# Optimization experiments

Hardware: AMD Instinct MI355X
Metric: run time of the kernel (lower is better)

The kernel has to match this reference:

```python
import jax, jax.numpy as jnp
import numpy as np

N = 131072      # num nodes
T = 16          # tile (block) size, tile_rows == tile_cols
BR = N // T     # block rows = 8192
K = 8           # nonzero blocks per block-row
IN_F, HID, NCLS = 128, 256, 64
LN_EPS = 1e-5


def setup_inputs() -> dict:
    key = jax.random.key(0)
    ks = jax.random.split(key, 8)
    features = jax.random.normal(ks[0], (N, IN_F), dtype=jnp.float32)
    block_vals = jax.random.uniform(ks[1], (BR, K, T, T), dtype=jnp.float32) / (K * T)
    block_cols = jax.random.randint(ks[2], (BR, K), 0, BR, dtype=jnp.int32)
    W0 = jax.random.normal(ks[3], (IN_F, HID), dtype=jnp.float32) / np.sqrt(IN_F)
    W1 = jax.random.normal(ks[4], (HID, HID), dtype=jnp.float32) / np.sqrt(HID)
    W2 = jax.random.normal(ks[5], (HID, NCLS), dtype=jnp.float32) / np.sqrt(HID)
    return {
        "features": features,
        "block_vals": block_vals,
        "W0": W0, "b0": jnp.zeros((HID,), jnp.float32),
        "W1": W1, "b1": jnp.zeros((HID,), jnp.float32),
        "W2": W2, "b2": jnp.zeros((NCLS,), jnp.float32),
        "g0": jnp.ones((HID,), jnp.float32), "beta0": jnp.zeros((HID,), jnp.float32),
        "g1": jnp.ones((HID,), jnp.float32), "beta1": jnp.zeros((HID,), jnp.float32),
        "block_cols": block_cols,
    }


def bcsr_spmm(block_vals, block_cols, z):
    """Block-CSR sparse matmul: out = A @ z.
    block_vals: [BR, K, T, T], block_cols: [BR, K] (block-column ids), z: [N, F]."""
    f = z.shape[-1]
    zb = z.reshape(BR, T, f)[block_cols]          # gather column blocks -> [BR, K, T, F]
    out = jnp.einsum('bkrc,bkcf->brf', block_vals, zb)  # block GEMM + accumulate over K
    return out.reshape(N, f)


def layer_norm(x, g, b):
    mu = jnp.mean(x, axis=-1, keepdims=True)
    var = jnp.mean(jnp.square(x - mu), axis=-1, keepdims=True)
    return g * (x - mu) * jax.lax.rsqrt(var + LN_EPS) + b


def reference(features, block_vals, W0, b0, W1, b1, W2, b2,
              g0, beta0, g1, beta1, block_cols):
    # layer 0: h' = A @ (h W0) + b0 ; relu ; LayerNorm
    h = bcsr_spmm(block_vals, block_cols, features @ W0) + b0
    h = layer_norm(jax.nn.relu(h), g0, beta0)
    # layer 1
    h = bcsr_spmm(block_vals, block_cols, h @ W1) + b1
    h = layer_norm(jax.nn.relu(h), g1, beta1)
    # output layer (no activation/norm)
    h = bcsr_spmm(block_vals, block_cols, h @ W2) + b2
    return h
```

## Files before the change

### kernel.cpp

```cpp
#include <hip/hip_runtime.h>
#include <hip/hip_bf16.h>


typedef __bf16 bf16;
typedef bf16 bf16x8 __attribute__((ext_vector_type(8)));
typedef bf16 bf16x4 __attribute__((ext_vector_type(4)));
typedef float f32x4 __attribute__((ext_vector_type(4)));

#define N_NODES 131072
#define BRQ 8192
#define KNZ 8
#define IN_F 128
#define HID 256
#define NCLS 64

static __device__ __forceinline__ f32x4 mfma16(bf16x8 a, bf16x8 b, f32x4 c) {
  return __builtin_amdgcn_mfma_f32_16x16x32_bf16(a, b, c, 0, 0, 0);
}

static __device__ __forceinline__ bf16x8 load8(const bf16* p) {
  return *(const bf16x8*)p;
}
static __device__ __forceinline__ bf16x8 load8(const float* p) {
  f32x4 a0 = *(const f32x4*)p;
  f32x4 a1 = *(const f32x4*)(p + 4);
  bf16x8 r;
  r[0] = (bf16)a0[0]; r[1] = (bf16)a0[1]; r[2] = (bf16)a0[2]; r[3] = (bf16)a0[3];
  r[4] = (bf16)a1[0]; r[5] = (bf16)a1[1]; r[6] = (bf16)a1[2]; r[7] = (bf16)a1[3];
  return r;
}

__global__ void transpose_all(const float* __restrict__ W0, const float* __restrict__ W1,
                              const float* __restrict__ W2, bf16* __restrict__ w0t,
                              bf16* __restrict__ w1t, bf16* __restrict__ w2t) {
  int idx = blockIdx.x * 256 + threadIdx.x;
  if (idx < 32768) {
    int r = idx >> 8, c = idx & 255;
    w0t[c * 128 + r] = (bf16)W0[idx];
  } else if (idx < 98304) {
    int j = idx - 32768; int r = j >> 8, c = j & 255;
    w1t[c * 256 + r] = (bf16)W1[j];
  } else {
    int j = idx - 98304; int r = j >> 6, c = j & 63;
    w2t[c * 256 + r] = (bf16)W2[j];
  }
}

template<typename TA, int KIN, int FOUT, int GRID>
__global__ __launch_bounds__(256) void gemm_bt(const TA* __restrict__ X,
                                               const bf16* __restrict__ WT,
                                               bf16* __restrict__ Zbt) {
  constexpr int CG  = FOUT / 64;
  constexpr int KS  = KIN / 32;
  constexpr int RTS = GRID * 4 / CG;
  constexpr int NT  = BRQ / RTS;

  const int wave = threadIdx.x >> 6;
  const int lane = threadIdx.x & 63;
  const int l15  = lane & 15;
  const int quad = lane >> 4;
  const int gw   = blockIdx.x * 4 + wave;
  const int cg   = gw % CG;
  const int rt0  = gw / CG;

  const bf16* __restrict__ wbase = WT + (long)(cg * 64 + l15) * KIN + quad * 8;
  bf16x8 bfr[KS][4];
#pragma unroll
  for (int k = 0; k < KS; ++k)
#pragma unroll
    for (int t = 0; t < 4; ++t)
      bfr[k][t] = *(const bf16x8*)(wbase + t * (16 * KIN) + k * 32);

  const TA* __restrict__ xbase = X + (long)l15 * KIN + quad * 8;

  bf16x8 aw[2][KS];
#pragma unroll
  for (int k = 0; k < KS; ++k)
    aw[0][k] = load8(xbase + (long)rt0 * (16 * KIN) + k * 32);

#pragma unroll
  for (int it = 0; it < NT; ++it) {
    const int rt = rt0 + it * RTS;
    if (it + 1 < NT) {
      const long xoff = (long)(rt + RTS) * (16 * KIN);
#pragma unroll
      for (int k = 0; k < KS; ++k)
        aw[(it + 1) & 1][k] = load8(xbase + xoff + k * 32);
    }
    f32x4 acc[4] = {};
#pragma unroll
    for (int k = 0; k < KS; ++k)
#pragma unroll
      for (int t = 0; t < 4; ++t)
        acc[t] = mfma16(aw[it & 1][k], bfr[k][t], acc[t]);
#pragma unroll
    for (int t = 0; t < 4; ++t) {
      int col = cg * 64 + t * 16 + l15;
      bf16x4 v;
#pragma unroll
      for (int i = 0; i < 4; ++i) v[i] = (bf16)acc[t][i];
      *(bf16x4*)(Zbt + ((long)rt * FOUT + col) * 16 + quad * 4) = v;
    }
  }
}

__global__ __launch_bounds__(256) void spmm_ln(const float* __restrict__ Abv,
                                               const int*   __restrict__ Abc,
                                               const bf16*  __restrict__ Zbt,
                                               const float* __restrict__ bias,
                                               const float* __restrict__ gamma,
                                               const float* __restrict__ beta,
                                               bf16* __restrict__ H) {
  const int wave = threadIdx.x >> 6;
  const int lane = threadIdx.x & 63;
  const int l15  = lane & 15;
  const int quad = lane >> 4;
  const int b    = blockIdx.x * 2 + (wave >> 1);
  const int ch   = wave & 1;

  const int*   bc    = Abc + b * KNZ;
  const int    cst   = (quad & 1) * 8;
  const int    half  = quad >> 1;
  const float* abase = Abv + (long)b * (KNZ * 256) + l15 * 16 + cst;

  bf16x8 afr[4];
  long   zb[4];
#pragma unroll
  for (int kp = 0; kp < 4; ++kp) {
    int blk = 2 * kp + half;
    afr[kp] = load8(abase + blk * 256);
    zb[kp]  = (long)bc[blk] * (HID * 16) + cst;
  }
  bf16x8 bfr[4][8];
#pragma unroll
  for (int kp = 0; kp < 4; ++kp)
#pragma unroll
    for (int t = 0; t < 8; ++t) {
      int f = ch * 128 + t * 16 + l15;
      bfr[kp][t] = *(const bf16x8*)(Zbt + zb[kp] + f * 16);
    }

  f32x4 acc[8] = {};
#pragma unroll
  for (int kp = 0; kp < 4; ++kp)
#pragma unroll
    for (int t = 0; t < 8; ++t)
      acc[t] = mfma16(afr[kp], bfr[kp][t], acc[t]);

  float gv[8], bv[8];
#pragma unroll
  for (int t = 0; t < 8; ++t) {
    int f = ch * 128 + t * 16 + l15;
    gv[t] = gamma[f];
    bv[t] = beta[f];
  }
  float ps[4] = {0.f, 0.f, 0.f, 0.f}, pss[4] = {0.f, 0.f, 0.f, 0.f};
#pragma unroll
  for (int t = 0; t < 8; ++t) {
    float bi = bias[ch * 128 + t * 16 + l15];
#pragma unroll
    for (int i = 0; i < 4; ++i) {
      float v = acc[t][i] + bi;
      v = v > 0.f ? v : 0.f;
      acc[t][i] = v;
      ps[i] += v;
      pss[i] += v * v;
    }
  }
#pragma unroll
  for (int m = 1; m < 16; m <<= 1) {
#pragma unroll
    for (int i = 0; i < 4; ++i) {
      ps[i]  += __shfl_xor(ps[i], m, 64);
      pss[i] += __shfl_xor(pss[i], m, 64);
    }
  }
  __shared__ float S[4][16], SS[4][16];
  if (l15 == 0) {
#pragma unroll
    for (int i = 0; i < 4; ++i) {
      S[wave][quad * 4 + i]  = ps[i];
      SS[wave][quad * 4 + i] = pss[i];
    }
  }
  __syncthreads();
#pragma unroll
  for (int i = 0; i < 4; ++i) {
    int r = quad * 4 + i;
    float s    = S[wave][r] + S[wave ^ 1][r];
    float ss   = SS[wave][r] + SS[wave ^ 1][r];
    float mu   = s * (1.f / 256.f);
    float var  = ss * (1.f / 256.f) - mu * mu;
    float rstd = rsqrtf(var + 1e-5f);
    bf16* hrow = H + (long)(b * 16 + r) * HID;
#pragma unroll
    for (int t = 0; t < 8; ++t) {
      int f = ch * 128 + t * 16 + l15;
      float y = (acc[t][i] - mu) * rstd * gv[t] + bv[t];
      hrow[f] = (bf16)y;
    }
  }
}

__global__ __launch_bounds__(256) void spmm_out(const float* __restrict__ Abv,
                                                const int*   __restrict__ Abc,
                                                const bf16*  __restrict__ Zbt,
                                                const float* __restrict__ bias,
                                                float* __restrict__ out) {
  const int wave = threadIdx.x >> 6;
  const int b    = blockIdx.x * 4 + wave;
  const int lane = threadIdx.x & 63;
  const int l15  = lane & 15;
  const int quad = lane >> 4;

  const int*   bc    = Abc + b * KNZ;
  const int    cst   = (quad & 1) * 8;
  const int    half  = quad >> 1;
  const float* abase = Abv + (long)b * (KNZ * 256) + l15 * 16 + cst;

  bf16x8 afr[4];
  long   zb[4];
#pragma unroll
  for (int kp = 0; kp < 4; ++kp) {
    int blk = 2 * kp + half;
    afr[kp] = load8(abase + blk * 256);
    zb[kp]  = (long)bc[blk] * (NCLS * 16) + cst;
  }
  bf16x8 bfr[4][4];
#pragma unroll
  for (int kp = 0; kp < 4; ++kp)
#pragma unroll
    for (int t = 0; t < 4; ++t) {
      int f = t * 16 + l15;
      bfr[kp][t] = *(const bf16x8*)(Zbt + zb[kp] + f * 16);
    }

  f32x4 acc[4] = {};
#pragma unroll
  for (int kp = 0; kp < 4; ++kp)
#pragma unroll
    for (int t = 0; t < 4; ++t)
      acc[t] = mfma16(afr[kp], bfr[kp][t], acc[t]);

#pragma unroll
  for (int t = 0; t < 4; ++t) {
    int f = t * 16 + l15;
    float bi = bias[f];
#pragma unroll
    for (int i = 0; i < 4; ++i) {
      out[(long)(b * 16 + quad * 4 + i) * NCLS + f] = acc[t][i] + bi;
    }
  }
}

extern "C" void kernel_launch(void* const* d_in, const int* in_sizes, int n_in,
                              void* d_out, int out_size, void* d_ws, size_t ws_size,
                              hipStream_t stream) {
  const float* features = (const float*)d_in[0];
  const float* bvals    = (const float*)d_in[1];
  const float* W0       = (const float*)d_in[2];
  const float* b0       = (const float*)d_in[3];
  const float* W1       = (const float*)d_in[4];
  const float* b1       = (const float*)d_in[5];
  const float* W2       = (const float*)d_in[6];
  const float* b2       = (const float*)d_in[7];
  const float* g0       = (const float*)d_in[8];
  const float* beta0    = (const float*)d_in[9];
  const float* g1       = (const float*)d_in[10];
  const float* beta1    = (const float*)d_in[11];
  const int*   bcols    = (const int*)d_in[12];
  float* outp = (float*)d_out;

  bf16* zbt = (bf16*)d_ws;
  bf16* h   = zbt + (size_t)N_NODES * HID;

  bf16* w0t = (bf16*)d_out;
  bf16* w1t = w0t + IN_F * HID;
  bf16* w2t = w1t + HID * HID;

  transpose_all<<<dim3(448), dim3(256), 0, stream>>>(W0, W1, W2, w0t, w1t, w2t);

  gemm_bt<float, IN_F, HID, 1024><<<dim3(1024), dim3(256), 0, stream>>>(features, w0t, zbt);
  spmm_ln<<<dim3(BRQ / 2), dim3(256), 0, stream>>>(bvals, bcols, zbt, b0, g0, beta0, h);
  gemm_bt<bf16, HID, HID, 1024><<<dim3(1024), dim3(256), 0, stream>>>(h, w1t, zbt);
  spmm_ln<<<dim3(BRQ / 2), dim3(256), 0, stream>>>(bvals, bcols, zbt, b1, g1, beta1, h);
  gemm_bt<bf16, HID, NCLS, 512><<<dim3(512), dim3(256), 0, stream>>>(h, w2t, zbt);
  spmm_out<<<dim3(BRQ / 4), dim3(256), 0, stream>>>(bvals, bcols, zbt, b2, outp);
}
```

Before: 462.7 us.

## Reorder layer-0 as (A@X)@W0, pre-convert block values to bf16, fuse LayerNorm into GEMM

Layer 0 now runs the block-sparse product on the 128-wide features first, then multiplies by W0. Because A is linear this gives the same result, and the gather-heavy SpMM works on half the width. The sparse block values are converted to bf16 once into the output buffer and shared by all three SpMMs, so the fp32 values are no longer re-read in each layer. Bias, ReLU and LayerNorm are fused into the layer-0 GEMM epilogue using a cross-wave shared-memory reduction with a barrier per tile. The separate weight-transpose kernel is removed: weights are read strided from fp32 and converted inside each GEMM. The costs are extra prep kernels and more complex buffer aliasing.

Result: no change. 468.0 us (+1.1%).

```diff
diff --git a/kernel.cpp b/kernel.cpp
--- a/kernel.cpp
+++ b/kernel.cpp
@@ -14,6 +14,8 @@
 #define HID 256
 #define NCLS 64
 
+#define SB() __builtin_amdgcn_sched_barrier(0)
+
 static __device__ __forceinline__ f32x4 mfma16(bf16x8 a, bf16x8 b, f32x4 c) {
   return __builtin_amdgcn_mfma_f32_16x16x32_bf16(a, b, c, 0, 0, 0);
 }
@@ -21,34 +23,93 @@
 static __device__ __forceinline__ bf16x8 load8(const bf16* p) {
   return *(const bf16x8*)p;
 }
-static __device__ __forceinline__ bf16x8 load8(const float* p) {
-  f32x4 a0 = *(const f32x4*)p;
-  f32x4 a1 = *(const f32x4*)(p + 4);
+static __device__ __forceinline__ bf16x8 cvt8(f32x4 a0, f32x4 a1) {
   bf16x8 r;
   r[0] = (bf16)a0[0]; r[1] = (bf16)a0[1]; r[2] = (bf16)a0[2]; r[3] = (bf16)a0[3];
   r[4] = (bf16)a1[0]; r[5] = (bf16)a1[1]; r[6] = (bf16)a1[2]; r[7] = (bf16)a1[3];
   return r;
 }
 
-__global__ void transpose_all(const float* __restrict__ W0, const float* __restrict__ W1,
-                              const float* __restrict__ W2, bf16* __restrict__ w0t,
-                              bf16* __restrict__ w1t, bf16* __restrict__ w2t) {
-  int idx = blockIdx.x * 256 + threadIdx.x;
-  if (idx < 32768) {
-    int r = idx >> 8, c = idx & 255;
-    w0t[c * 128 + r] = (bf16)W0[idx];
-  } else if (idx < 98304) {
-    int j = idx - 32768; int r = j >> 8, c = j & 255;
-    w1t[c * 256 + r] = (bf16)W1[j];
-  } else {
-    int j = idx - 98304; int r = j >> 6, c = j & 63;
-    w2t[c * 256 + r] = (bf16)W2[j];
-  }
-}
-
-template<typename TA, int KIN, int FOUT, int GRID>
-__global__ __launch_bounds__(256) void gemm_bt(const TA* __restrict__ X,
-                                               const bf16* __restrict__ WT,
+__global__ __launch_bounds__(256) void prep_bvals(const float* __restrict__ V,
+                                                  bf16* __restrict__ Ab) {
+  long i = ((long)blockIdx.x * 256 + threadIdx.x) * 8;
+  f32x4 a0 = *(const f32x4*)(V + i);
+  f32x4 a1 = *(const f32x4*)(V + i + 4);
+  *(bf16x8*)(Ab + i) = cvt8(a0, a1);
+}
+
+__global__ __launch_bounds__(256) void prep_fbt(const float* __restrict__ F,
+                                                bf16* __restrict__ out) {
+  __shared__ float T[16][132];
+  const int b = blockIdx.x, tid = threadIdx.x;
+#pragma unroll
+  for (int p = 0; p < 2; ++p) {
+    int ci = tid + p * 256;
+    int r = ci >> 5, c4 = ci & 31;
+    f32x4 v = *(const f32x4*)(F + ((long)b * 16 + r) * 128 + c4 * 4);
+    *(f32x4*)&T[r][c4 * 4] = v;
+  }
+  __syncthreads();
+  int f = tid >> 1, r0 = (tid & 1) * 8;
+  bf16x8 o;
+#pragma unroll
+  for (int e = 0; e < 8; ++e) o[e] = (bf16)T[r0 + e][f];
+  *(bf16x8*)(out + (long)b * 2048 + f * 16 + r0) = o;
+}
+
+__global__ __launch_bounds__(256) void spmm_f(const bf16* __restrict__ Ab,
+                                              const int*  __restrict__ Abc,
+                                              const bf16* __restrict__ Fbt,
+                                              bf16* __restrict__ S0) {
+  const int wave = threadIdx.x >> 6;
+  const int b    = blockIdx.x * 4 + wave;
+  const int lane = threadIdx.x & 63;
+  const int l15  = lane & 15;
+  const int quad = lane >> 4;
+  const int cst  = (quad & 1) * 8;
+  const int half = quad >> 1;
+
+  const int*  bc    = Abc + b * KNZ;
+  const bf16* abase = Ab + (long)b * (KNZ * 256) + l15 * 16 + cst;
+
+  bf16x8 afr[4];
+  long   zb[4];
+#pragma unroll
+  for (int kp = 0; kp < 4; ++kp) {
+    int blk = 2 * kp + half;
+    afr[kp] = load8(abase + blk * 256);
+    zb[kp]  = (long)bc[blk] * (IN_F * 16) + cst;
+  }
+  bf16x8 bfr[4][8];
+#pragma unroll
+  for (int kp = 0; kp < 4; ++kp)
+#pragma unroll
+    for (int t = 0; t < 8; ++t) {
+      int f = t * 16 + l15;
+      bfr[kp][t] = *(const bf16x8*)(Fbt + zb[kp] + f * 16);
+    }
+
+  f32x4 acc[8] = {};
+#pragma unroll
+  for (int kp = 0; kp < 4; ++kp)
+#pragma unroll
+    for (int t = 0; t < 8; ++t)
+      acc[t] = mfma16(afr[kp], bfr[kp][t], acc[t]);
+
+#pragma unroll
+  for (int t = 0; t < 8; ++t)
+#pragma unroll
+    for (int i = 0; i < 4; ++i)
+      S0[((long)b * 16 + quad * 4 + i) * IN_F + t * 16 + l15] = (bf16)acc[t][i];
+}
+
+template<int KIN, int FOUT, int GRID, bool LN>
+__global__ __launch_bounds__(256) void gemm_ln(const bf16*  __restrict__ X,
+                                               const float* __restrict__ W,
+                                               const float* __restrict__ bias,
+                                               const float* __restrict__ gamma,
+                                               const float* __restrict__ beta,
+                                               bf16* __restrict__ Hrow,
                                                bf16* __restrict__ Zbt) {
   constexpr int CG  = FOUT / 64;
   constexpr int KS  = KIN / 32;
@@ -63,15 +124,29 @@
   const int cg   = gw % CG;
   const int rt0  = gw / CG;
 
-  const bf16* __restrict__ wbase = WT + (long)(cg * 64 + l15) * KIN + quad * 8;
-  bf16x8 bfr[KS][4];
+  bf16x8 wbf[KS][4];
 #pragma unroll
   for (int k = 0; k < KS; ++k)
 #pragma unroll
-    for (int t = 0; t < 4; ++t)
-      bfr[k][t] = *(const bf16x8*)(wbase + t * (16 * KIN) + k * 32);
-
-  const TA* __restrict__ xbase = X + (long)l15 * KIN + quad * 8;
+    for (int t = 0; t < 4; ++t) {
+      const float* wp = W + (long)(k * 32 + quad * 8) * FOUT + cg * 64 + t * 16 + l15;
+      bf16x8 v;
+#pragma unroll
+      for (int j = 0; j < 8; ++j) v[j] = (bf16)wp[(long)j * FOUT];
+      wbf[k][t] = v;
+    }
+  float bv[4], gv[4], btv[4];
+  if constexpr (LN) {
+#pragma unroll
+    for (int t = 0; t < 4; ++t) {
+      int col = cg * 64 + t * 16 + l15;
+      bv[t] = bias[col]; gv[t] = gamma[col]; btv[t] = beta[col];
+    }
+  }
+
+  __shared__ float S[2][4][16], SS[2][4][16];
+
+  const bf16* __restrict__ xbase = X + (long)l15 * KIN + quad * 8;
 
   bf16x8 aw[2][KS];
 #pragma unroll
@@ -92,19 +167,65 @@
     for (int k = 0; k < KS; ++k)
 #pragma unroll
       for (int t = 0; t < 4; ++t)
-        acc[t] = mfma16(aw[it & 1][k], bfr[k][t], acc[t]);
-#pragma unroll
-    for (int t = 0; t < 4; ++t) {
-      int col = cg * 64 + t * 16 + l15;
-      bf16x4 v;
-#pragma unroll
-      for (int i = 0; i < 4; ++i) v[i] = (bf16)acc[t][i];
-      *(bf16x4*)(Zbt + ((long)rt * FOUT + col) * 16 + quad * 4) = v;
-    }
-  }
-}
-
-__global__ __launch_bounds__(256) void spmm_ln(const float* __restrict__ Abv,
+        acc[t] = mfma16(aw[it & 1][k], wbf[k][t], acc[t]);
+
+    if constexpr (LN) {
+      float ps[4] = {0.f, 0.f, 0.f, 0.f}, pss[4] = {0.f, 0.f, 0.f, 0.f};
+#pragma unroll
+      for (int t = 0; t < 4; ++t)
+#pragma unroll
+        for (int i = 0; i < 4; ++i) {
+          float v = acc[t][i] + bv[t];
+          v = v > 0.f ? v : 0.f;
+          acc[t][i] = v;
+          ps[i] += v;
+          pss[i] += v * v;
+        }
+#pragma unroll
+      for (int m = 1; m < 16; m <<= 1)
+#pragma unroll
+        for (int i = 0; i < 4; ++i) {
+          ps[i]  += __shfl_xor(ps[i], m, 64);
+          pss[i] += __shfl_xor(pss[i], m, 64);
+        }
+      const int par = it & 1;
+      if (l15 == 0)
+#pragma unroll
+        for (int i = 0; i < 4; ++i) {
+          S[par][wave][quad * 4 + i]  = ps[i];
+          SS[par][wave][quad * 4 + i] = pss[i];
+        }
+      SB();
+      asm volatile("s_waitcnt lgkmcnt(0)" ::: "memory");
+      __builtin_amdgcn_s_barrier();
+      SB();
+#pragma unroll
+      for (int i = 0; i < 4; ++i) {
+        int r = quad * 4 + i;
+        float s  = S[par][0][r] + S[par][1][r] + S[par][2][r] + S[par][3][r];
+        float ss = SS[par][0][r] + SS[par][1][r] + SS[par][2][r] + SS[par][3][r];
+        float mu   = s * (1.f / FOUT);
+        float var  = ss * (1.f / FOUT) - mu * mu;
+        float rstd = rsqrtf(var + 1e-5f);
+        bf16* hrow = Hrow + ((long)rt * 16 + r) * FOUT + cg * 64;
+#pragma unroll
+        for (int t = 0; t < 4; ++t)
+          hrow[t * 16 + l15] = (bf16)((acc[t][i] - mu) * rstd * gv[t] + btv[t]);
+      }
+    } else {
+#pragma unroll
+      for (int t = 0; t < 4; ++t) {
+        int col = cg * 64 + t * 16 + l15;
+        bf16x4 v;
+#pragma unroll
+        for (int i = 0; i < 4; ++i) v[i] = (bf16)acc[t][i];
+        *(bf16x4*)(Zbt + ((long)rt * FOUT + col) * 16 + quad * 4) = v;
+      }
+    }
+  }
+}
+
+__global__ __launch_bounds__(256) void spmm_ln(const bf16*  __restrict__ Abv,
                                                const int*   __restrict__ Abc,
                                                const bf16*  __restrict__ Zbt,
                                                const float* __restrict__ bias,
@@ -118,10 +239,10 @@
   const int b    = blockIdx.x * 2 + (wave >> 1);
   const int ch   = wave & 1;
 
-  const int*   bc    = Abc + b * KNZ;
-  const int    cst   = (quad & 1) * 8;
-  const int    half  = quad >> 1;
-  const float* abase = Abv + (long)b * (KNZ * 256) + l15 * 16 + cst;
+  const int*  bc    = Abc + b * KNZ;
+  const int   cst   = (quad & 1) * 8;
+  const int   half  = quad >> 1;
+  const bf16* abase = Abv + (long)b * (KNZ * 256) + l15 * 16 + cst;
 
   bf16x8 afr[4];
   long   zb[4];
@@ -202,7 +323,7 @@
   }
 }
 
-__global__ __launch_bounds__(256) void spmm_out(const float* __restrict__ Abv,
+__global__ __launch_bounds__(256) void spmm_out(const bf16*  __restrict__ Abv,
                                                 const int*   __restrict__ Abc,
                                                 const bf16*  __restrict__ Zbt,
                                                 const float* __restrict__ bias,
@@ -213,10 +334,10 @@
   const int l15  = lane & 15;
   const int quad = lane >> 4;
 
-  const int*   bc    = Abc + b * KNZ;
-  const int    cst   = (quad & 1) * 8;
-  const int    half  = quad >> 1;
-  const float* abase = Abv + (long)b * (KNZ * 256) + l15 * 16 + cst;
+  const int*  bc    = Abc + b * KNZ;
+  const int   cst   = (quad & 1) * 8;
+  const int   half  = quad >> 1;
+  const bf16* abase = Abv + (long)b * (KNZ * 256) + l15 * 16 + cst;
 
   bf16x8 afr[4];
   long   zb[4];
@@ -259,11 +380,11 @@
   const float* features = (const float*)d_in[0];
   const float* bvals    = (const float*)d_in[1];
   const float* W0       = (const float*)d_in[2];
-  const float* b0       = (const float*)d_in[3];
+  const float* b0v      = (const float*)d_in[3];
   const float* W1       = (const float*)d_in[4];
-  const float* b1       = (const float*)d_in[5];
+  const float* b1v      = (const float*)d_in[5];
   const float* W2       = (const float*)d_in[6];
-  const float* b2       = (const float*)d_in[7];
+  const float* b2v      = (const float*)d_in[7];
   const float* g0       = (const float*)d_in[8];
   const float* beta0    = (const float*)d_in[9];
   const float* g1       = (const float*)d_in[10];
@@ -271,19 +392,26 @@
   const int*   bcols    = (const int*)d_in[12];
   float* outp = (float*)d_out;
 
-  bf16* zbt = (bf16*)d_ws;
-  bf16* h   = zbt + (size_t)N_NODES * HID;
-
-  bf16* w0t = (bf16*)d_out;
-  bf16* w1t = w0t + IN_F * HID;
-  bf16* w2t = w1t + HID * HID;
-
-  transpose_all<<<dim3(448), dim3(256), 0, stream>>>(W0, W1, W2, w0t, w1t, w2t);
-
-  gemm_bt<float, IN_F, HID, 1024><<<dim3(1024), dim3(256), 0, stream>>>(features, w0t, zbt);
-  spmm_ln<<<dim3(BRQ / 2), dim3(256), 0, stream>>>(bvals, bcols, zbt, b0, g0, beta0, h);
-  gemm_bt<bf16, HID, HID, 1024><<<dim3(1024), dim3(256), 0, stream>>>(h, w1t, zbt);
-  spmm_ln<<<dim3(BRQ / 2), dim3(256), 0, stream>>>(bvals, bcols, zbt, b1, g1, beta1, h);
-  gemm_bt<bf16, HID, NCLS, 512><<<dim3(512), dim3(256), 0, stream>>>(h, w2t, zbt);
-  spmm_out<<<dim3(BRQ / 4), dim3(256), 0, stream>>>(bvals, bcols, zbt, b2, outp);
-}
+  char* ws = (char*)d_ws;
+  bf16* fbt  = (bf16*)ws;
+  bf16* S0   = (bf16*)(ws + (64L << 20));
+  bf16* h0   = (bf16*)ws;
+  bf16* zbt1 = (bf16*)(ws + (64L << 20));
+  bf16* h1   = (bf16*)ws;
+  bf16* zbt2 = (bf16*)(ws + (64L << 20));
+
+  bf16* Ab = (bf16*)d_out;
+
+  prep_bvals<<<dim3(BRQ), dim3(256), 0, stream>>>(bvals, Ab);
+  prep_fbt<<<dim3(BRQ), dim3(256), 0, stream>>>(features, fbt);
+
+  spmm_f<<<dim3(BRQ / 4), dim3(256), 0, stream>>>(Ab, bcols, fbt, S0);
+  gemm_ln<IN_F, HID, 1024, true><<<dim3(1024), dim3(256), 0, stream>>>(
+      S0, W0, b0v, g0, beta0, h0, nullptr);
+  gemm_ln<HID, HID, 1024, false><<<dim3(1024), dim3(256), 0, stream>>>(
+      h0, W1, nullptr, nullptr, nullptr, nullptr, zbt1);
+  spmm_ln<<<dim3(BRQ / 2), dim3(256), 0, stream>>>(Ab, bcols, zbt1, b1v, g1, beta1, h1);
+  gemm_ln<HID, NCLS, 512, false><<<dim3(512), dim3(256), 0, stream>>>(
+      h1, W2, nullptr, nullptr, nullptr, nullptr, zbt2);
+  spmm_out<<<dim3(BRQ / 4), dim3(256), 0, stream>>>(Ab, bcols, zbt2, b2v, outp);
+}
```

## Convert adjacency blocks to bf16 once and fold weight transpose into GEMMs

Applied to the files above, without the earlier changes.

The fp32 block values are now converted to bf16 once, inside extra workgroups appended to the first GEMM launch, and stored in the output buffer. All three SpMM kernels then read the half-size bf16 copy instead of re-reading fp32, which cuts their memory traffic. The separate weight-transpose kernel is removed: each GEMM loads fp32 weights with strided reads and converts them in registers, saving one launch. The risks are spmm_out reading Ab from the same output buffer it writes (each wave overwrites only the region it has already read), and uncoalesced strided weight loads.

Result: slower. 490.3 us (+6.0%).

```diff
diff --git a/kernel.cpp b/kernel.cpp
--- a/kernel.cpp
+++ b/kernel.cpp
@@ -21,55 +21,47 @@
 static __device__ __forceinline__ bf16x8 load8(const bf16* p) {
   return *(const bf16x8*)p;
 }
-static __device__ __forceinline__ bf16x8 load8(const float* p) {
-  f32x4 a0 = *(const f32x4*)p;
-  f32x4 a1 = *(const f32x4*)(p + 4);
+static __device__ __forceinline__ bf16x8 cvt8(f32x4 a0, f32x4 a1) {
   bf16x8 r;
   r[0] = (bf16)a0[0]; r[1] = (bf16)a0[1]; r[2] = (bf16)a0[2]; r[3] = (bf16)a0[3];
   r[4] = (bf16)a1[0]; r[5] = (bf16)a1[1]; r[6] = (bf16)a1[2]; r[7] = (bf16)a1[3];
   return r;
 }
-
-__global__ void transpose_all(const float* __restrict__ W0, const float* __restrict__ W1,
-                              const float* __restrict__ W2, bf16* __restrict__ w0t,
-                              bf16* __restrict__ w1t, bf16* __restrict__ w2t) {
-  int idx = blockIdx.x * 256 + threadIdx.x;
-  if (idx < 32768) {
-    int r = idx >> 8, c = idx & 255;
-    w0t[c * 128 + r] = (bf16)W0[idx];
-  } else if (idx < 98304) {
-    int j = idx - 32768; int r = j >> 8, c = j & 255;
-    w1t[c * 256 + r] = (bf16)W1[j];
-  } else {
-    int j = idx - 98304; int r = j >> 6, c = j & 63;
-    w2t[c * 256 + r] = (bf16)W2[j];
-  }
+static __device__ __forceinline__ bf16x8 load8(const float* p) {
+  f32x4 a0 = *(const f32x4*)p;
+  f32x4 a1 = *(const f32x4*)(p + 4);
+  return cvt8(a0, a1);
 }
 
 template<typename TA, int KIN, int FOUT, int GRID>
-__global__ __launch_bounds__(256) void gemm_bt(const TA* __restrict__ X,
-                                               const bf16* __restrict__ WT,
-                                               bf16* __restrict__ Zbt) {
+static __device__ __forceinline__ void gemm_body(int wgid, int tid,
+                                                 const TA* __restrict__ X,
+                                                 const float* __restrict__ W,
+                                                 bf16* __restrict__ Zbt) {
   constexpr int CG  = FOUT / 64;
   constexpr int KS  = KIN / 32;
   constexpr int RTS = GRID * 4 / CG;
   constexpr int NT  = BRQ / RTS;
 
-  const int wave = threadIdx.x >> 6;
-  const int lane = threadIdx.x & 63;
+  const int wave = tid >> 6;
+  const int lane = tid & 63;
   const int l15  = lane & 15;
   const int quad = lane >> 4;
-  const int gw   = blockIdx.x * 4 + wave;
+  const int gw   = wgid * 4 + wave;
   const int cg   = gw % CG;
   const int rt0  = gw / CG;
 
-  const bf16* __restrict__ wbase = WT + (long)(cg * 64 + l15) * KIN + quad * 8;
-  bf16x8 bfr[KS][4];
+  bf16x8 wbf[KS][4];
 #pragma unroll
   for (int k = 0; k < KS; ++k)
 #pragma unroll
-    for (int t = 0; t < 4; ++t)
-      bfr[k][t] = *(const bf16x8*)(wbase + t * (16 * KIN) + k * 32);
+    for (int t = 0; t < 4; ++t) {
+      const float* wp = W + (long)(k * 32 + quad * 8) * FOUT + cg * 64 + t * 16 + l15;
+      bf16x8 v;
+#pragma unroll
+      for (int j = 0; j < 8; ++j) v[j] = (bf16)wp[(long)j * FOUT];
+      wbf[k][t] = v;
+    }
 
   const TA* __restrict__ xbase = X + (long)l15 * KIN + quad * 8;
 
@@ -92,7 +84,7 @@
     for (int k = 0; k < KS; ++k)
 #pragma unroll
       for (int t = 0; t < 4; ++t)
-        acc[t] = mfma16(aw[it & 1][k], bfr[k][t], acc[t]);
+        acc[t] = mfma16(aw[it & 1][k], wbf[k][t], acc[t]);
 #pragma unroll
     for (int t = 0; t < 4; ++t) {
       int col = cg * 64 + t * 16 + l15;
@@ -104,7 +96,29 @@
   }
 }
 
-__global__ __launch_bounds__(256) void spmm_ln(const float* __restrict__ Abv,
+__global__ __launch_bounds__(256) void gemm0_prep(const float* __restrict__ X,
+                                                  const float* __restrict__ W,
+                                                  bf16* __restrict__ Zbt,
+                                                  const float* __restrict__ V,
+                                                  bf16* __restrict__ Ab) {
+  if (blockIdx.x < 1024) {
+    gemm_body<float, IN_F, HID, 1024>(blockIdx.x, threadIdx.x, X, W, Zbt);
+  } else {
+    long i = ((long)(blockIdx.x - 1024) * 256 + threadIdx.x) * 8;
+    f32x4 a0 = *(const f32x4*)(V + i);
+    f32x4 a1 = *(const f32x4*)(V + i + 4);
+    *(bf16x8*)(Ab + i) = cvt8(a0, a1);
+  }
+}
+
+template<int KIN, int FOUT, int GRID>
+__global__ __launch_bounds__(256) void gemm_bt2(const bf16* __restrict__ X,
+                                                const float* __restrict__ W,
+                                                bf16* __restrict__ Zbt) {
+  gemm_body<bf16, KIN, FOUT, GRID>(blockIdx.x, threadIdx.x, X, W, Zbt);
+}
+
+__global__ __launch_bounds__(256) void spmm_ln(const bf16*  __restrict__ Abv,
                                                const int*   __restrict__ Abc,
                                                const bf16*  __restrict__ Zbt,
                                                const float* __restrict__ bias,
@@ -118,10 +132,10 @@
   const int b    = blockIdx.x * 2 + (wave >> 1);
   const int ch   = wave & 1;
 
-  const int*   bc    = Abc + b * KNZ;
-  const int    cst   = (quad & 1) * 8;
-  const int    half  = quad >> 1;
-  const float* abase = Abv + (long)b * (KNZ * 256) + l15 * 16 + cst;
+  const int*  bc    = Abc + b * KNZ;
+  const int   cst   = (quad & 1) * 8;
+  const int   half  = quad >> 1;
+  const bf16* abase = Abv + (long)b * (KNZ * 256) + l15 * 16 + cst;
 
   bf16x8 afr[4];
   long   zb[4];
@@ -202,7 +216,7 @@
   }
 }
 
-__global__ __launch_bounds__(256) void spmm_out(const float* __restrict__ Abv,
+__global__ __launch_bounds__(256) void spmm_out(const bf16*  __restrict__ Abv,
                                                 const int*   __restrict__ Abc,
                                                 const bf16*  __restrict__ Zbt,
                                                 const float* __restrict__ bias,
@@ -213,10 +227,10 @@
   const int l15  = lane & 15;
   const int quad = lane >> 4;
 
-  const int*   bc    = Abc + b * KNZ;
-  const int    cst   = (quad & 1) * 8;
-  const int    half  = quad >> 1;
-  const float* abase = Abv + (long)b * (KNZ * 256) + l15 * 16 + cst;
+  const int*  bc    = Abc + b * KNZ;
+  const int   cst   = (quad & 1) * 8;
+  const int   half  = quad >> 1;
+  const bf16* abase = Abv + (long)b * (KNZ * 256) + l15 * 16 + cst;
 
   bf16x8 afr[4];
   long   zb[4];
@@ -259,11 +273,11 @@
   const float* features = (const float*)d_in[0];
   const float* bvals    = (const float*)d_in[1];
   const float* W0       = (const float*)d_in[2];
-  const float* b0       = (const float*)d_in[3];
+  const float* b0v      = (const float*)d_in[3];
   const float* W1       = (const float*)d_in[4];
-  const float* b1       = (const float*)d_in[5];
+  const float* b1v      = (const float*)d_in[5];
   const float* W2       = (const float*)d_in[6];
-  const float* b2       = (const float*)d_in[7];
+  const float* b2v      = (const float*)d_in[7];
   const float* g0       = (const float*)d_in[8];
   const float* beta0    = (const float*)d_in[9];
   const float* g1       = (const float*)d_in[10];
@@ -271,19 +285,19 @@
   const int*   bcols    = (const int*)d_in[12];
   float* outp = (float*)d_out;
 
-  bf16* zbt = (bf16*)d_ws;
-  bf16* h   = zbt + (size_t)N_NODES * HID;
-
-  bf16* w0t = (bf16*)d_out;
-  bf16* w1t = w0t + IN_F * HID;
-  bf16* w2t = w1t + HID * HID;
-
-  transpose_all<<<dim3(448), dim3(256), 0, stream>>>(W0, W1, W2, w0t, w1t, w2t);
-
-  gemm_bt<float, IN_F, HID, 1024><<<dim3(1024), dim3(256), 0, stream>>>(features, w0t, zbt);
-  spmm_ln<<<dim3(BRQ / 2), dim3(256), 0, stream>>>(bvals, bcols, zbt, b0, g0, beta0, h);
-  gemm_bt<bf16, HID, HID, 1024><<<dim3(1024), dim3(256), 0, stream>>>(h, w1t, zbt);
-  spmm_ln<<<dim3(BRQ / 2), dim3(256), 0, stream>>>(bvals, bcols, zbt, b1, g1, beta1, h);
-  gemm_bt<bf16, HID, NCLS, 512><<<dim3(512), dim3(256), 0, stream>>>(h, w2t, zbt);
-  spmm_out<<<dim3(BRQ / 4), dim3(256), 0, stream>>>(bvals, bcols, zbt, b2, outp);
-}
+  char* ws = (char*)d_ws;
+  bf16* zbt0 = (bf16*)(ws + (64L << 20));
+  bf16* h0   = (bf16*)ws;
+  bf16* zbt1 = (bf16*)(ws + (64L << 20));
+  bf16* h1   = (bf16*)ws;
+  bf16* zbt2 = (bf16*)(ws + (64L << 20));
+
+  bf16* Ab = (bf16*)d_out;
+
+  gemm0_prep<<<dim3(1024 + BRQ), dim3(256), 0, stream>>>(features, W0, zbt0, bvals, Ab);
+  spmm_ln<<<dim3(BRQ / 2), dim3(256), 0, stream>>>(Ab, bcols, zbt0, b0v, g0, beta0, h0);
+  gemm_bt2<HID, HID, 1024><<<dim3(1024), dim3(256), 0, stream>>>(h0, W1, zbt1);
+  spmm_ln<<<dim3(BRQ / 2), dim3(256), 0, stream>>>(Ab, bcols, zbt1, b1v, g1, beta1, h1);
+  gemm_bt2<HID, NCLS, 512><<<dim3(512), dim3(256), 0, stream>>>(h1, W2, zbt2);
+  spmm_out<<<dim3(BRQ / 4), dim3(256), 0, stream>>>(Ab, bcols, zbt2, b2v, outp);
+}
```
